# Optimization experiments

Measured on AMD Instinct MI355X. Metric: run time of the kernel, lower is better.

Reference implementation:

```python
import jax, jax.numpy as jnp
import numpy as np

B, T, C = 8, 2048, 1024   # batch, seq_len, n_embd
H = 128                   # head_size

def setup_inputs() -> dict:
    key = jax.random.key(0)
    kx, kk, kq, kv = jax.random.split(key, 4)
    scale = 1.0 / np.sqrt(C)
    return {
        "x": jax.random.normal(kx, (B, T, C), dtype=jnp.float32),
        "Wk": jax.random.normal(kk, (C, H), dtype=jnp.float32) * scale,
        "Wq": jax.random.normal(kq, (C, H), dtype=jnp.float32) * scale,
        "Wv": jax.random.normal(kv, (C, H), dtype=jnp.float32) * scale,
    }

def reference(x, Wk, Wq, Wv):
    # k,q,v: [B,T,H]
    k = x @ Wk
    q = x @ Wq
    v = x @ Wv
    # NOTE: original scales by C**-0.5 (n_embd), not head_size**-0.5
    wei = jnp.einsum("bth,bsh->bts", q, k) * (x.shape[-1] ** -0.5)  # [B,T,T]
    wei = jax.nn.softmax(wei, axis=-1)  # no causal mask in the source module
    # dropout = 0.0 -> identity
    out = jnp.einsum("bts,bsh->bth", wei, v)  # [B,T,H]
    return out
```

## Files before the change

kernel.cpp:

```cpp
#include <hip/hip_runtime.h>
#include <hip/hip_bf16.h>
#include <stdint.h>
#include <stddef.h>

#define NB 8
#define NT 2048
#define NC 1024
#define NH 128

typedef float f32x4 __attribute__((ext_vector_type(4)));
typedef short bf16x8 __attribute__((ext_vector_type(8)));

__device__ __forceinline__ unsigned short f2bf(float f) {
    union { float f; uint32_t u; } v; v.f = f;
    uint32_t u = v.u;
    u += 0x7fffu + ((u >> 16) & 1u);
    return (unsigned short)(u >> 16);
}

__device__ __forceinline__ void gld16(const void* gp, void* lp) {
    __builtin_amdgcn_global_load_lds(
        (const __attribute__((address_space(1))) unsigned int*)gp,
        (__attribute__((address_space(3))) unsigned int*)lp, 16, 0, 0);
}


__global__ __launch_bounds__(256) void cast_w_kernel(const float* __restrict__ Wq,
                                                     const float* __restrict__ Wk,
                                                     const float* __restrict__ Wv,
                                                     unsigned short* __restrict__ Wtf) {
    int gid  = blockIdx.x * 256 + threadIdx.x;
    int lane = gid & 63;
    int fs   = gid >> 6;
    int kb   = fs & 31;
    int g    = fs >> 5;
    int w    = g >> 3;
    int g16  = g & 7;
    int quad = lane >> 4;
    int l16  = lane & 15;
    const float* src = (w == 0) ? Wq : ((w == 1) ? Wk : Wv);
    int n = g16 * 16 + l16;
    bf16x8 o;
#pragma unroll
    for (int j = 0; j < 8; ++j)
        o[j] = (short)f2bf(src[(size_t)(kb * 32 + quad * 8 + j) * 128 + n]);
    *(bf16x8*)(Wtf + (size_t)gid * 8) = o;
}

#define CS2 392

__global__ __launch_bounds__(256, 2) void proj_kernel(const float* __restrict__ x,
                                                      const unsigned short* __restrict__ Wtf,
                                                      unsigned short* __restrict__ Qf,
                                                      unsigned short* __restrict__ Kf,
                                                      unsigned short* __restrict__ Vf) {
    __shared__ __align__(16) unsigned short wbuf[2][24 * 512];

    const int tid  = threadIdx.x;
    const int wave = tid >> 6;
    const int lane = tid & 63;
    const int quad = lane >> 4;
    const int l16  = lane & 15;
    const int bidx = blockIdx.x;
    const int rowbase = bidx * 32;
    const int b    = bidx >> 6;
    const int mt   = wave & 1;
    const int nh   = wave >> 1;

    const float* xrow = x + (size_t)(rowbase + mt * 16 + l16) * NC;

    auto stageW = [&](int kb, int bi) {
#pragma unroll
        for (int i = 0; i < 6; ++i) {
            const int g = wave * 6 + i;
            gld16(Wtf + ((size_t)(g * 32 + kb) * 512) + lane * 8, &wbuf[bi][g * 512]);
        }
    };

    stageW(0, 0);
    __syncthreads();

    f32x4 acc[12] = {};
    for (int kb = 0; kb < 32; ++kb) {
        const int cur = kb & 1;
        if (kb < 31) stageW(kb + 1, cur ^ 1);
        const float* src = xrow + kb * 32 + quad * 8;
        float4 f0 = *(const float4*)src;
        float4 f1 = *(const float4*)(src + 4);
        bf16x8 a;
        a[0] = (short)f2bf(f0.x); a[1] = (short)f2bf(f0.y);
        a[2] = (short)f2bf(f0.z); a[3] = (short)f2bf(f0.w);
        a[4] = (short)f2bf(f1.x); a[5] = (short)f2bf(f1.y);
        a[6] = (short)f2bf(f1.z); a[7] = (short)f2bf(f1.w);
#pragma unroll
        for (int i = 0; i < 12; ++i) {
            bf16x8 wf = *(const bf16x8*)(&wbuf[cur][(nh * 12 + i) * 512 + lane * 8]);
            acc[i] = __builtin_amdgcn_mfma_f32_16x16x32_bf16(a, wf, acc[i], 0, 0, 0);
        }
        __syncthreads();
    }

    unsigned short* cs = (unsigned short*)wbuf;
#pragma unroll
    for (int i = 0; i < 12; ++i) {
        const int g = nh * 12 + i;
#pragma unroll
        for (int r = 0; r < 4; ++r)
            cs[(mt * 16 + quad * 4 + r) * CS2 + g * 16 + l16] = f2bf(acc[i][r]);
    }
    __syncthreads();

    const int ibase = (rowbase & (NT - 1)) >> 4;
    const int tc    = (rowbase & (NT - 1)) >> 5;
    unsigned short* qdst = Qf + (size_t)b * (NT * NH);
    unsigned short* kdst = Kf + (size_t)b * (NT * NH);
    unsigned short* vdst = Vf + (size_t)b * (NT * NH);

    {
        const int mq   = wave & 1;
        const int isK  = wave >> 1;
        unsigned short* dst = isK ? kdst : qdst;
        const int off = isK * 128;
        const int iqt = ibase + mq;
#pragma unroll
        for (int ks = 0; ks < 4; ++ks) {
            bf16x8 v = *(const bf16x8*)(&cs[(mq * 16 + l16) * CS2 + off + ks * 32 + quad * 8]);
            *(bf16x8*)(dst + ((size_t)(iqt * 4 + ks) * 64 + lane) * 8) = v;
        }
    }
#pragma unroll
    for (int i = 0; i < 2; ++i) {
        const int nt = wave * 2 + i;
        bf16x8 v;
#pragma unroll
        for (int j = 0; j < 8; ++j)
            v[j] = (short)cs[(quad * 8 + j) * CS2 + 256 + nt * 16 + l16];
        *(bf16x8*)(vdst + ((size_t)(nt * 64 + tc) * 64 + lane) * 8) = v;
    }
}

__global__ __launch_bounds__(256, 2) void attn_kernel(const unsigned short* __restrict__ Qf,
                                                      const unsigned short* __restrict__ Kf,
                                                      const unsigned short* __restrict__ Vf,
                                                      float* __restrict__ out) {
    __shared__ __align__(16) unsigned short kbuf[2][16 * 512];
    __shared__ __align__(16) unsigned short vbuf[2][16 * 512];
    __shared__ __align__(16) unsigned short p_all[4][16 * 40];
    __shared__ float sl[4][16];

    const int tid  = threadIdx.x;
    const int wave = tid >> 6;
    const int lane = tid & 63;
    const int quad = lane >> 4;
    const int l16  = lane & 15;
    const int bid  = blockIdx.x;
    const int b    = bid & 7;
    const int iqb  = bid >> 3;
    const int mt   = wave & 1;
    const int kh   = wave >> 1;
    const int iq   = iqb * 2 + mt;

    const unsigned short* qfp = Qf + (size_t)b * (NT * NH);
    const unsigned short* kfp = Kf + (size_t)b * (NT * NH);
    const unsigned short* vfp = Vf + (size_t)b * (NT * NH);
    unsigned short* p_w = p_all[wave];

    bf16x8 qf[4];
#pragma unroll
    for (int ks = 0; ks < 4; ++ks)
        qf[ks] = *(const bf16x8*)(qfp + ((size_t)(iq * 4 + ks) * 64 + lane) * 8);

    auto stage = [&](int j, int bi) {
#pragma unroll
        for (int i = 0; i < 8; ++i) {
            const int fid = wave * 8 + i;
            if (fid < 16) {
                gld16(kfp + ((size_t)(j * 16 + fid) * 512) + lane * 8, &kbuf[bi][fid * 512]);
            } else {
                const int s  = fid - 16;
                const int nt = s >> 1;
                const int c  = s & 1;
                gld16(vfp + ((size_t)(nt * 64 + j * 2 + c) * 512) + lane * 8, &vbuf[bi][s * 512]);
            }
        }
    };

    stage(0, 0);
    __syncthreads();

    f32x4 O[8] = {};
    float lsum[4] = {0.f, 0.f, 0.f, 0.f};
    const float scl2 = 0.03125f * 1.44269504088896340736f;

    for (int j = 0; j < 32; ++j) {
        const int cur = j & 1;
        if (j < 31) stage(j + 1, cur ^ 1);

        f32x4 S[2] = {};
#pragma unroll
        for (int ks = 0; ks < 4; ++ks) {
            bf16x8 kf0 = *(const bf16x8*)(&kbuf[cur][((kh * 2 + 0) * 4 + ks) * 512 + lane * 8]);
            bf16x8 kf1 = *(const bf16x8*)(&kbuf[cur][((kh * 2 + 1) * 4 + ks) * 512 + lane * 8]);
            S[0] = __builtin_amdgcn_mfma_f32_16x16x32_bf16(qf[ks], kf0, S[0], 0, 0, 0);
            S[1] = __builtin_amdgcn_mfma_f32_16x16x32_bf16(qf[ks], kf1, S[1], 0, 0, 0);
        }

#pragma unroll
        for (int n2 = 0; n2 < 2; ++n2) {
#pragma unroll
            for (int r = 0; r < 4; ++r) {
                float p = __builtin_amdgcn_exp2f(S[n2][r] * scl2);
                lsum[r] += p;
                p_w[(quad * 4 + r) * 40 + n2 * 16 + l16] = f2bf(p);
            }
        }

        bf16x8 pf = *(const bf16x8*)(&p_w[l16 * 40 + quad * 8]);
#pragma unroll
        for (int nt = 0; nt < 8; ++nt) {
            bf16x8 vf = *(const bf16x8*)(&vbuf[cur][(nt * 2 + kh) * 512 + lane * 8]);
            O[nt] = __builtin_amdgcn_mfma_f32_16x16x32_bf16(pf, vf, O[nt], 0, 0, 0);
        }

        __syncthreads();
    }

#pragma unroll
    for (int msk = 1; msk <= 8; msk <<= 1) {
#pragma unroll
        for (int r = 0; r < 4; ++r)
            lsum[r] += __shfl_xor(lsum[r], msk, 64);
    }

    if (l16 == 0) {
#pragma unroll
        for (int r = 0; r < 4; ++r)
            sl[wave][quad * 4 + r] = lsum[r];
    }
    float* so = (float*)kbuf;
    if (wave >= 2) {
#pragma unroll
        for (int nt = 0; nt < 8; ++nt) {
#pragma unroll
            for (int r = 0; r < 4; ++r)
                so[((size_t)(wave - 2) * 16 + quad * 4 + r) * 132 + nt * 16 + l16] = O[nt][r];
        }
    }
    __syncthreads();

    if (wave < 2) {
        float inv[4];
#pragma unroll
        for (int r = 0; r < 4; ++r)
            inv[r] = 1.0f / (sl[wave][quad * 4 + r] + sl[wave + 2][quad * 4 + r]);
        float* orow = out + ((size_t)b * NT + iq * 16) * NH;
#pragma unroll
        for (int nt = 0; nt < 8; ++nt) {
#pragma unroll
            for (int r = 0; r < 4; ++r) {
                float v = O[nt][r] + so[((size_t)wave * 16 + quad * 4 + r) * 132 + nt * 16 + l16];
                orow[(quad * 4 + r) * NH + nt * 16 + l16] = v * inv[r];
            }
        }
    }
}

extern "C" void kernel_launch(void* const* d_in, const int* in_sizes, int n_in,
                              void* d_out, int out_size, void* d_ws, size_t ws_size,
                              hipStream_t stream) {
    const float* x  = (const float*)d_in[0];
    const float* Wk = (const float*)d_in[1];
    const float* Wq = (const float*)d_in[2];
    const float* Wv = (const float*)d_in[3];
    float* out = (float*)d_out;

    char* ws = (char*)d_ws;
    unsigned short* Qf  = (unsigned short*)(ws);
    unsigned short* Kf  = (unsigned short*)(ws + 4194304);
    unsigned short* Vf  = (unsigned short*)(ws + 8388608);
    unsigned short* Wtf = (unsigned short*)(ws + 12582912);

    cast_w_kernel<<<192, 256, 0, stream>>>(Wq, Wk, Wv, Wtf);
    proj_kernel<<<512, 256, 0, stream>>>(x, Wtf, Qf, Kf, Vf);
    attn_kernel<<<512, 256, 0, stream>>>(Qf, Kf, Vf, out);
}
```

Before: 176.9 us.

## Restructure attention to load K/V directly from global with 8-wave blocks; stage x in LDS

The attention kernel drops the LDS double-buffered K/V staging. It launches 256 blocks of 512 threads, where each wave handles one query tile and half the key range. K and V fragments are read directly from global memory, larger 128-key chunks are computed per iteration, and P is stored in a per-wave LDS buffer. The projection kernel now stages x through a padded bf16 LDS buffer instead of converting per-lane global loads. This trades LDS staging and barriers for more global/L2 traffic and register pressure; the barrier inside the attention loop appears unnecessary.

```diff
diff --git a/kernel.cpp b/kernel.cpp
--- a/kernel.cpp
+++ b/kernel.cpp
@@ -10,6 +10,7 @@
 
 typedef float f32x4 __attribute__((ext_vector_type(4)));
 typedef short bf16x8 __attribute__((ext_vector_type(8)));
+typedef short bf16x4 __attribute__((ext_vector_type(4)));
 
 __device__ __forceinline__ unsigned short f2bf(float f) {
     union { float f; uint32_t u; } v; v.f = f;
@@ -48,6 +49,7 @@
 }
 
 #define CS2 392
+#define XP  34
 
 __global__ __launch_bounds__(256, 2) void proj_kernel(const float* __restrict__ x,
                                                       const unsigned short* __restrict__ Wtf,
@@ -55,6 +57,7 @@
                                                       unsigned short* __restrict__ Kf,
                                                       unsigned short* __restrict__ Vf) {
     __shared__ __align__(16) unsigned short wbuf[2][24 * 512];
+    __shared__ __align__(16) unsigned short xbuf[2][32 * XP];
 
     const int tid  = threadIdx.x;
     const int wave = tid >> 6;
@@ -67,8 +70,15 @@
     const int mt   = wave & 1;
     const int nh   = wave >> 1;
 
-    const float* xrow = x + (size_t)(rowbase + mt * 16 + l16) * NC;
-
+    auto stageX = [&](int kb, int bi) {
+        const int row = tid >> 3;
+        const int ko  = (tid & 7) * 4;
+        float4 f = *(const float4*)(x + (size_t)(rowbase + row) * NC + kb * 32 + ko);
+        bf16x4 o;
+        o[0] = (short)f2bf(f.x); o[1] = (short)f2bf(f.y);
+        o[2] = (short)f2bf(f.z); o[3] = (short)f2bf(f.w);
+        *(bf16x4*)(&xbuf[bi][row * XP + ko]) = o;
+    };
     auto stageW = [&](int kb, int bi) {
 #pragma unroll
         for (int i = 0; i < 6; ++i) {
@@ -77,21 +87,18 @@
         }
     };
 
+    stageX(0, 0);
     stageW(0, 0);
     __syncthreads();
 
     f32x4 acc[12] = {};
     for (int kb = 0; kb < 32; ++kb) {
         const int cur = kb & 1;
-        if (kb < 31) stageW(kb + 1, cur ^ 1);
-        const float* src = xrow + kb * 32 + quad * 8;
-        float4 f0 = *(const float4*)src;
-        float4 f1 = *(const float4*)(src + 4);
-        bf16x8 a;
-        a[0] = (short)f2bf(f0.x); a[1] = (short)f2bf(f0.y);
-        a[2] = (short)f2bf(f0.z); a[3] = (short)f2bf(f0.w);
-        a[4] = (short)f2bf(f1.x); a[5] = (short)f2bf(f1.y);
-        a[6] = (short)f2bf(f1.z); a[7] = (short)f2bf(f1.w);
+        if (kb < 31) {
+            stageX(kb + 1, cur ^ 1);
+            stageW(kb + 1, cur ^ 1);
+        }
+        bf16x8 a = *(const bf16x8*)(&xbuf[cur][(mt * 16 + l16) * XP + quad * 8]);
 #pragma unroll
         for (int i = 0; i < 12; ++i) {
             bf16x8 wf = *(const bf16x8*)(&wbuf[cur][(nh * 12 + i) * 512 + lane * 8]);
@@ -139,126 +146,113 @@
     }
 }
 
-__global__ __launch_bounds__(256, 2) void attn_kernel(const unsigned short* __restrict__ Qf,
+__global__ __launch_bounds__(512, 2) void attn_kernel(const unsigned short* __restrict__ Qf,
                                                       const unsigned short* __restrict__ Kf,
                                                       const unsigned short* __restrict__ Vf,
                                                       float* __restrict__ out) {
-    __shared__ __align__(16) unsigned short kbuf[2][16 * 512];
-    __shared__ __align__(16) unsigned short vbuf[2][16 * 512];
-    __shared__ __align__(16) unsigned short p_all[4][16 * 40];
-    __shared__ float sl[4][16];
+    __shared__ __align__(16) unsigned char smem[34816];
+    __shared__ float sl[2][4][16];
 
     const int tid  = threadIdx.x;
     const int wave = tid >> 6;
     const int lane = tid & 63;
     const int quad = lane >> 4;
     const int l16  = lane & 15;
+    const int h    = wave & 1;
+    const int m    = wave >> 1;
     const int bid  = blockIdx.x;
     const int b    = bid & 7;
-    const int iqb  = bid >> 3;
-    const int mt   = wave & 1;
-    const int kh   = wave >> 1;
-    const int iq   = iqb * 2 + mt;
+    const int iq   = (bid >> 3) * 4 + m;
+
+    unsigned short* p_w = (unsigned short*)smem + wave * 16 * 136;
+    float* so = (float*)smem;
 
     const unsigned short* qfp = Qf + (size_t)b * (NT * NH);
     const unsigned short* kfp = Kf + (size_t)b * (NT * NH);
     const unsigned short* vfp = Vf + (size_t)b * (NT * NH);
-    unsigned short* p_w = p_all[wave];
 
     bf16x8 qf[4];
 #pragma unroll
     for (int ks = 0; ks < 4; ++ks)
         qf[ks] = *(const bf16x8*)(qfp + ((size_t)(iq * 4 + ks) * 64 + lane) * 8);
-
-    auto stage = [&](int j, int bi) {
-#pragma unroll
-        for (int i = 0; i < 8; ++i) {
-            const int fid = wave * 8 + i;
-            if (fid < 16) {
-                gld16(kfp + ((size_t)(j * 16 + fid) * 512) + lane * 8, &kbuf[bi][fid * 512]);
-            } else {
-                const int s  = fid - 16;
-                const int nt = s >> 1;
-                const int c  = s & 1;
-                gld16(vfp + ((size_t)(nt * 64 + j * 2 + c) * 512) + lane * 8, &vbuf[bi][s * 512]);
-            }
-        }
-    };
-
-    stage(0, 0);
-    __syncthreads();
 
     f32x4 O[8] = {};
     float lsum[4] = {0.f, 0.f, 0.f, 0.f};
     const float scl2 = 0.03125f * 1.44269504088896340736f;
 
-    for (int j = 0; j < 32; ++j) {
-        const int cur = j & 1;
-        if (j < 31) stage(j + 1, cur ^ 1);
-
-        f32x4 S[2] = {};
+    for (int j = 0; j < 8; ++j) {
+        const int kt = h * 8 + j;
+
+        f32x4 S[8] = {};
 #pragma unroll
         for (int ks = 0; ks < 4; ++ks) {
-            bf16x8 kf0 = *(const bf16x8*)(&kbuf[cur][((kh * 2 + 0) * 4 + ks) * 512 + lane * 8]);
-            bf16x8 kf1 = *(const bf16x8*)(&kbuf[cur][((kh * 2 + 1) * 4 + ks) * 512 + lane * 8]);
-            S[0] = __builtin_amdgcn_mfma_f32_16x16x32_bf16(qf[ks], kf0, S[0], 0, 0, 0);
-            S[1] = __builtin_amdgcn_mfma_f32_16x16x32_bf16(qf[ks], kf1, S[1], 0, 0, 0);
-        }
-
-#pragma unroll
-        for (int n2 = 0; n2 < 2; ++n2) {
+            bf16x8 kf[8];
+#pragma unroll
+            for (int nt = 0; nt < 8; ++nt)
+                kf[nt] = *(const bf16x8*)(kfp + ((size_t)((kt * 8 + nt) * 4 + ks) * 64 + lane) * 8);
+#pragma unroll
+            for (int nt = 0; nt < 8; ++nt)
+                S[nt] = __builtin_amdgcn_mfma_f32_16x16x32_bf16(qf[ks], kf[nt], S[nt], 0, 0, 0);
+        }
+
+#pragma unroll
+        for (int nt = 0; nt < 8; ++nt) {
 #pragma unroll
             for (int r = 0; r < 4; ++r) {
-                float p = __builtin_amdgcn_exp2f(S[n2][r] * scl2);
+                float p = __builtin_amdgcn_exp2f(S[nt][r] * scl2);
                 lsum[r] += p;
-                p_w[(quad * 4 + r) * 40 + n2 * 16 + l16] = f2bf(p);
+                p_w[(quad * 4 + r) * 136 + nt * 16 + l16] = f2bf(p);
             }
         }
 
-        bf16x8 pf = *(const bf16x8*)(&p_w[l16 * 40 + quad * 8]);
+#pragma unroll
+        for (int k2 = 0; k2 < 4; ++k2) {
+            bf16x8 vf[8];
+#pragma unroll
+            for (int nt = 0; nt < 8; ++nt)
+                vf[nt] = *(const bf16x8*)(vfp + ((size_t)(nt * 64 + kt * 4 + k2) * 64 + lane) * 8);
+            bf16x8 pf = *(const bf16x8*)(&p_w[l16 * 136 + k2 * 32 + quad * 8]);
+#pragma unroll
+            for (int nt = 0; nt < 8; ++nt)
+                O[nt] = __builtin_amdgcn_mfma_f32_16x16x32_bf16(pf, vf[nt], O[nt], 0, 0, 0);
+        }
+
+        __syncthreads();
+    }
+
+#pragma unroll
+    for (int msk = 1; msk <= 8; msk <<= 1) {
+#pragma unroll
+        for (int r = 0; r < 4; ++r)
+            lsum[r] += __shfl_xor(lsum[r], msk, 64);
+    }
+    if (l16 == 0) {
+#pragma unroll
+        for (int r = 0; r < 4; ++r)
+            sl[h][m][quad * 4 + r] = lsum[r];
+    }
+    __syncthreads();
+    if (h == 1) {
 #pragma unroll
         for (int nt = 0; nt < 8; ++nt) {
-            bf16x8 vf = *(const bf16x8*)(&vbuf[cur][(nt * 2 + kh) * 512 + lane * 8]);
-            O[nt] = __builtin_amdgcn_mfma_f32_16x16x32_bf16(pf, vf, O[nt], 0, 0, 0);
-        }
-
-        __syncthreads();
-    }
-
-#pragma unroll
-    for (int msk = 1; msk <= 8; msk <<= 1) {
-#pragma unroll
-        for (int r = 0; r < 4; ++r)
-            lsum[r] += __shfl_xor(lsum[r], msk, 64);
-    }
-
-    if (l16 == 0) {
-#pragma unroll
-        for (int r = 0; r < 4; ++r)
-            sl[wave][quad * 4 + r] = lsum[r];
-    }
-    float* so = (float*)kbuf;
-    if (wave >= 2) {
+#pragma unroll
+            for (int r = 0; r < 4; ++r)
+                so[((size_t)m * 16 + quad * 4 + r) * 132 + nt * 16 + l16] = O[nt][r];
+        }
+    }
+    __syncthreads();
+
+    if (h == 0) {
+        float inv[4];
+#pragma unroll
+        for (int r = 0; r < 4; ++r)
+            inv[r] = 1.0f / (sl[0][m][quad * 4 + r] + sl[1][m][quad * 4 + r]);
+        float* orow = out + ((size_t)b * NT + iq * 16) * NH;
 #pragma unroll
         for (int nt = 0; nt < 8; ++nt) {
 #pragma unroll
-            for (int r = 0; r < 4; ++r)
-                so[((size_t)(wave - 2) * 16 + quad * 4 + r) * 132 + nt * 16 + l16] = O[nt][r];
-        }
-    }
-    __syncthreads();
-
-    if (wave < 2) {
-        float inv[4];
-#pragma unroll
-        for (int r = 0; r < 4; ++r)
-            inv[r] = 1.0f / (sl[wave][quad * 4 + r] + sl[wave + 2][quad * 4 + r]);
-        float* orow = out + ((size_t)b * NT + iq * 16) * NH;
-#pragma unroll
-        for (int nt = 0; nt < 8; ++nt) {
-#pragma unroll
             for (int r = 0; r < 4; ++r) {
-                float v = O[nt][r] + so[((size_t)wave * 16 + quad * 4 + r) * 132 + nt * 16 + l16];
+                float v = O[nt][r] + so[((size_t)m * 16 + quad * 4 + r) * 132 + nt * 16 + l16];
                 orow[(quad * 4 + r) * NH + nt * 16 + l16] = v * inv[r];
             }
         }
@@ -282,5 +276,5 @@
 
     cast_w_kernel<<<192, 256, 0, stream>>>(Wq, Wk, Wv, Wtf);
     proj_kernel<<<512, 256, 0, stream>>>(x, Wtf, Qf, Kf, Vf);
-    attn_kernel<<<512, 256, 0, stream>>>(Qf, Kf, Vf, out);
-}
+    attn_kernel<<<256, 512, 0, stream>>>(Qf, Kf, Vf, out);
+}
```

Measured after the change: 227.5 us. 1.29x slower.
